# Kernel optimization log

Hardware: AMD Instinct MI355X
Metric: run time of the kernel (lower is better)

Reference implementation:

```python
import jax, jax.numpy as jnp
import numpy as np


def _min_gru_layer(h_in, Wz, bz, Wh, bh):
    # h_in: [B, T, D_in]; gates/candidate via two GEMMs
    z = jax.nn.sigmoid(jnp.einsum('btd,dh->bth', h_in, Wz) + bz)  # [B,T,H]
    h_tilde = jnp.einsum('btd,dh->bth', h_in, Wh) + bh            # [B,T,H]
    # Recurrence h_t = a_t * h_{t-1} + b_t with a_t = 1-z_t, b_t = z_t*h_tilde.
    # h_0 = 0 (frozen zeros param in the torch module), so the associative
    # scan over (a, b) directly yields h_t for t = 1..T.
    a = 1.0 - z
    b = z * h_tilde

    def combine(c1, c2):
        a1, b1 = c1
        a2, b2 = c2
        return a1 * a2, a2 * b1 + b2

    _, h = jax.lax.associative_scan(combine, (a, b), axis=1)
    return h


def setup_inputs() -> dict:
    key = jax.random.key(0)
    ks = jax.random.split(key, 8)
    B, T, Din, H, Dout = 8, 4096, 512, 1024, 512
    s_in = 1.0 / np.sqrt(Din)
    s_h = 1.0 / np.sqrt(H)
    return {
        'x':   jax.random.normal(ks[0], (B, T, Din), dtype=jnp.float32),
        'Wz0': jax.random.normal(ks[1], (Din, H), dtype=jnp.float32) * s_in,
        'bz0': jnp.zeros((H,), dtype=jnp.float32),
        'Wh0': jax.random.normal(ks[2], (Din, H), dtype=jnp.float32) * s_in,
        'bh0': jnp.zeros((H,), dtype=jnp.float32),
        'Wz1': jax.random.normal(ks[3], (H, H), dtype=jnp.float32) * s_h,
        'bz1': jnp.zeros((H,), dtype=jnp.float32),
        'Wh1': jax.random.normal(ks[4], (H, H), dtype=jnp.float32) * s_h,
        'bh1': jnp.zeros((H,), dtype=jnp.float32),
        'Wfc': jax.random.normal(ks[5], (H, Dout), dtype=jnp.float32) * s_h,
        'bfc': jnp.zeros((Dout,), dtype=jnp.float32),
    }


def reference(x, Wz0, bz0, Wh0, bh0, Wz1, bz1, Wh1, bh1, Wfc, bfc):
    h = _min_gru_layer(x, Wz0, bz0, Wh0, bh0)   # layer 0
    h = _min_gru_layer(h, Wz1, bz1, Wh1, bh1)   # layer 1
    return jnp.einsum('bth,ho->bto', h, Wfc) + bfc
```

## Files before the change

kernel.cpp:

```cpp
#include <hip/hip_runtime.h>

typedef __attribute__((ext_vector_type(4))) float fv4;
typedef __attribute__((ext_vector_type(8))) _Float16 hv8;
typedef __attribute__((ext_vector_type(4))) _Float16 hv4;
typedef __attribute__((ext_vector_type(2))) _Float16 hv2;

__device__ __forceinline__ void gload16(const void* g, void* l) {
  __builtin_amdgcn_global_load_lds(
      (const __attribute__((address_space(1))) unsigned int*)g,
      (__attribute__((address_space(3))) unsigned int*)l, 16, 0, 0);
}

struct GemmCore256 {
  const _Float16 *ap, *bp;
  size_t rstep;
  _Float16* ls;
  const _Float16 *fa, *fb;
  int wv;

  __device__ __forceinline__ void init(const _Float16* A, const _Float16* Bt,
                                       _Float16* lds, int m0, int n0, int K,
                                       int tid) {
    ls = lds;
    wv = tid >> 6;
    const int lane = tid & 63;
    const int wm = wv >> 2, wn = wv & 3;
    const int quad = lane >> 4, r = lane & 15;
    const int cg = (tid & 3) ^ ((tid >> 3) & 3);
    ap = A  + (size_t)(m0 + (tid >> 2)) * K + cg * 8;
    bp = Bt + (size_t)(n0 + (tid >> 2)) * K + cg * 8;
    rstep = (size_t)128 * K;
    const int sq = quad ^ ((r >> 1) & 3);
    fa = ls + (wm * 128 + r) * 32 + sq * 8;
    fb = ls + 8192 + (wn * 64 + r) * 32 + sq * 8;
  }

  __device__ __forceinline__ void stage4(int s) {
    _Float16* d = ls + (s & 3) * 16384 + wv * 512;
    const _Float16* a = ap + (size_t)s * 32;
    const _Float16* b = bp + (size_t)s * 32;
    gload16(a,         d);
    gload16(a + rstep, d + 4096);
    gload16(b,         d + 8192);
    gload16(b + rstep, d + 12288);
  }

  template <int VM, bool STAGE>
  __device__ __forceinline__ void body(fv4 acc[8][4], int s) {
    __builtin_amdgcn_s_barrier();
    __builtin_amdgcn_sched_barrier(0);
    if (STAGE) stage4(s + 3);
    const _Float16* fA = fa + (s & 3) * 16384;
    const _Float16* fB = fb + (s & 3) * 16384;
    hv8 a0[8], b0[4];
#pragma unroll
    for (int t = 0; t < 4; ++t) a0[t] = *(const hv8*)(fA + t * 512);
#pragma unroll
    for (int t = 0; t < 4; ++t) b0[t] = *(const hv8*)(fB + t * 512);
#pragma unroll
    for (int t = 0; t < 4; ++t) a0[t + 4] = *(const hv8*)(fA + (t + 4) * 512);
    __builtin_amdgcn_s_setprio(1);
#pragma unroll
    for (int tm = 0; tm < 4; ++tm)
#pragma unroll
      for (int tn = 0; tn < 4; ++tn)
        acc[tm][tn] = __builtin_amdgcn_mfma_f32_16x16x32_f16(a0[tm], b0[tn],
                                                             acc[tm][tn], 0, 0, 0);
#pragma unroll
    for (int tm = 0; tm < 4; ++tm)
#pragma unroll
      for (int tn = 0; tn < 4; ++tn)
        acc[tm + 4][tn] = __builtin_amdgcn_mfma_f32_16x16x32_f16(a0[tm + 4], b0[tn],
                                                                 acc[tm + 4][tn], 0, 0, 0);
    __builtin_amdgcn_s_setprio(0);
    if constexpr (VM >= 0)
      asm volatile("s_waitcnt vmcnt(%0)" :: "n"(VM) : "memory");
  }

  __device__ __forceinline__ void run(fv4 acc[8][4], int K) {
    const int ns = K >> 5;
    stage4(0); stage4(1); stage4(2);
    asm volatile("s_waitcnt vmcnt(8)" ::: "memory");
    int s = 0;
    for (; s < ns - 3; ++s) body<8, true>(acc, s);
    body<4, false>(acc, s); ++s;
    body<0, false>(acc, s); ++s;
    body<-1, false>(acc, s);
  }
};

__device__ __forceinline__ void xcd_map(int bid, int ntl2, int mt_per_x,
                                        int& m0, int& n0) {
  const int xcd = bid & 7;
  const int k2  = bid >> 3;
  m0 = (xcd * mt_per_x + (k2 >> ntl2)) * 256;
  n0 = (k2 & ((1 << ntl2) - 1)) * 256;
}

__global__ __launch_bounds__(512, 2)
void gemm_gate(const _Float16* __restrict__ A, const _Float16* __restrict__ Btf,
               _Float16* __restrict__ zh2,
               float* __restrict__ cA, float* __restrict__ cB,
               const float* __restrict__ bz, const float* __restrict__ bh,
               int K, int ntl2, int mt_per_x) {
  __shared__ _Float16 lds[4 * 16384];
  const int tid  = threadIdx.x;
  const int lane = tid & 63;
  const int wave = tid >> 6;
  const int wm = wave >> 2, wn = wave & 3;
  const int quad = lane >> 4, r = lane & 15;
  int m0, n0;
  xcd_map(blockIdx.x, ntl2, mt_per_x, m0, n0);

  GemmCore256 core;
  core.init(A, Btf, lds, m0, n0, K, tid);
  fv4 acc[8][4] = {};
  core.run(acc, K);

  const int jb   = (n0 + wn * 64) >> 1;
  const int row0 = m0 + wm * 128 + quad * 4;
  const int cb   = (m0 >> 6) + wm * 2;
#pragma unroll
  for (int tn = 0; tn < 2; ++tn) {
    const int j = jb + tn * 16 + r;
    const float bzv = bz[j];
    const float bhv = bh[j];
#pragma unroll
    for (int tg = 0; tg < 2; ++tg) {
      float qA[4], qB[4];
#pragma unroll
      for (int tq = 0; tq < 4; ++tq) {
        const int tm = tg * 4 + tq;
        float sA = 1.0f, sB = 0.0f;
#pragma unroll
        for (int r2 = 0; r2 < 4; ++r2) {
          const float zpre = acc[tm][tn][r2] + bzv;
          const float hpre = acc[tm][tn + 2][r2] + bhv;
          const float z = 1.0f / (1.0f + __expf(-zpre));
          const _Float16 a16 = (_Float16)(1.0f - z);
          const _Float16 b16 = (_Float16)(z * hpre);
          hv2 ab = {a16, b16};
          *(hv2*)(zh2 + ((size_t)(row0 + tm * 16 + r2) * 1024 + j) * 2) = ab;
          const float af = (float)a16, bf = (float)b16;
          sB = af * sB + bf;
          sA = sA * af;
        }
        qA[tq] = sA; qB[tq] = sB;
      }
#pragma unroll
      for (int tq = 0; tq < 4; ++tq) {
        float Av = qA[tq], Bv = qB[tq];
        float Ap = __shfl_up(Av, 16, 64);
        float Bp = __shfl_up(Bv, 16, 64);
        if (quad >= 1) { Bv = Av * Bp + Bv; Av = Ap * Av; }
        Ap = __shfl_up(Av, 32, 64);
        Bp = __shfl_up(Bv, 32, 64);
        if (quad >= 2) { Bv = Av * Bp + Bv; Av = Ap * Av; }
        qA[tq] = Av; qB[tq] = Bv;
      }
      if (quad == 3) {
        float CA = 1.0f, CB = 0.0f;
#pragma unroll
        for (int tq = 0; tq < 4; ++tq) { CB = qA[tq] * CB + qB[tq]; CA *= qA[tq]; }
        cA[(size_t)(cb + tg) * 1024 + j] = CA;
        cB[(size_t)(cb + tg) * 1024 + j] = CB;
      }
    }
  }
}

__global__ __launch_bounds__(512, 2)
void gemm_f16_bt(const _Float16* __restrict__ A, const _Float16* __restrict__ Bt,
                 float* __restrict__ C, const float* __restrict__ bias,
                 int N, int K, int ntl2, int mt_per_x) {
  __shared__ _Float16 lds[4 * 16384];
  const int tid  = threadIdx.x;
  const int lane = tid & 63;
  const int wave = tid >> 6;
  const int wm = wave >> 2, wn = wave & 3;
  const int quad = lane >> 4, r = lane & 15;
  int m0, n0;
  xcd_map(blockIdx.x, ntl2, mt_per_x, m0, n0);

  GemmCore256 core;
  core.init(A, Bt, lds, m0, n0, K, tid);
  fv4 acc[8][4] = {};
  core.run(acc, K);

  const int col0 = n0 + wn * 64 + r;
  const int row0 = m0 + wm * 128 + quad * 4;
#pragma unroll
  for (int tn = 0; tn < 4; ++tn) {
    const int col = col0 + tn * 16;
    const float bs = bias[col];
#pragma unroll
    for (int tm = 0; tm < 8; ++tm) {
#pragma unroll
      for (int r2 = 0; r2 < 4; ++r2) {
        C[(size_t)(row0 + tm * 16 + r2) * N + col] = acc[tm][tn][r2] + bs;
      }
    }
  }
}

__global__ void cvt_f16(const float* __restrict__ x, _Float16* __restrict__ y) {
  size_t i = ((size_t)blockIdx.x * 256 + threadIdx.x) * 4;
  fv4 v = *(const fv4*)(x + i);
  *(hv4*)(y + i) = __builtin_convertvector(v, hv4);
}

__global__ void transpose_cvt(const float* __restrict__ W, _Float16* __restrict__ Wt,
                              int K, int N, int mult, int off) {
  __shared__ float tile[32][33];
  const int tx = threadIdx.x, ty = threadIdx.y;
  const int n  = blockIdx.x * 32 + tx;
  const int kb = blockIdx.y * 32;
  for (int i = ty; i < 32; i += 8)
    tile[i][tx] = W[(size_t)(kb + i) * N + n];
  __syncthreads();
  const int k = kb + tx;
  for (int i = ty; i < 32; i += 8)
    Wt[(size_t)(blockIdx.x * mult + off + i) * K + k] = (_Float16)tile[tx][i];
}

__global__ void scan_phaseB(const float* __restrict__ cA, const float* __restrict__ cB,
                            float* __restrict__ hcy) {
  const int gtid = blockIdx.x * 256 + threadIdx.x;
  const int lane = gtid & 63;
  const int wid  = gtid >> 6;
  const int h  = (wid & 255) * 4;
  const int bb = wid >> 8;
  const size_t o = (size_t)(bb * 64 + lane) * 1024 + h;
  fv4 Aa = *(const fv4*)(cA + o);
  fv4 Bv = *(const fv4*)(cB + o);
#pragma unroll
  for (int d = 1; d < 64; d <<= 1) {
    fv4 Ap, Bp;
#pragma unroll
    for (int k = 0; k < 4; ++k) {
      Ap[k] = __shfl_up(Aa[k], d, 64);
      Bp[k] = __shfl_up(Bv[k], d, 64);
    }
    if (lane >= d) {
      Bv = Aa * Bp + Bv;
      Aa = Ap * Aa;
    }
  }
  fv4 hc;
#pragma unroll
  for (int k = 0; k < 4; ++k) hc[k] = __shfl_up(Bv[k], 1, 64);
  if (lane == 0) { hc.x = 0.f; hc.y = 0.f; hc.z = 0.f; hc.w = 0.f; }
  *(fv4*)(hcy + o) = hc;
}

__global__ void scan_phaseC(const _Float16* __restrict__ zh2,
                            const float* __restrict__ hcy,
                            _Float16* __restrict__ hout) {
  const int idx = blockIdx.x * 256 + threadIdx.x;
  const int h  = (idx & 255) * 4;
  const int c  = (idx >> 8) & 63;
  const int bb = idx >> 14;
  const size_t base = ((size_t)(bb * 4096 + c * 64) * 1024 + h) * 2;
  const size_t ob   = (size_t)(bb * 4096 + c * 64) * 1024 + h;
  const size_t o    = (size_t)(bb * 64 + c) * 1024 + h;
  fv4 hc = *(const fv4*)(hcy + o);
#pragma unroll 4
  for (int t = 0; t < 64; ++t) {
    hv8 v = *(const hv8*)(zh2 + base + (size_t)t * 2048);
    fv4 av = __builtin_convertvector(__builtin_shufflevector(v, v, 0, 2, 4, 6), fv4);
    fv4 bv = __builtin_convertvector(__builtin_shufflevector(v, v, 1, 3, 5, 7), fv4);
    hc = av * hc + bv;
    *(hv4*)(hout + ob + (size_t)t * 1024) = __builtin_convertvector(hc, hv4);
  }
}

extern "C" void kernel_launch(void* const* d_in, const int* in_sizes, int n_in,
                              void* d_out, int out_size, void* d_ws, size_t ws_size,
                              hipStream_t stream) {
  const float* x   = (const float*)d_in[0];
  const float* Wz0 = (const float*)d_in[1];
  const float* bz0 = (const float*)d_in[2];
  const float* Wh0 = (const float*)d_in[3];
  const float* bh0 = (const float*)d_in[4];
  const float* Wz1 = (const float*)d_in[5];
  const float* bz1 = (const float*)d_in[6];
  const float* Wh1 = (const float*)d_in[7];
  const float* bh1 = (const float*)d_in[8];
  const float* Wfc = (const float*)d_in[9];
  const float* bfc = (const float*)d_in[10];

  const int Mrows = 32768;
  const int H = 1024, Din = 512, Dout = 512;

  char* w = (char*)d_ws;
  _Float16* zh2   = (_Float16*)w; w += (size_t)Mrows * 2 * H * 2;
  _Float16* hx    = (_Float16*)w; w += (size_t)Mrows * H * 2;
  _Float16* Wzh0t = (_Float16*)w; w += (size_t)2 * H * Din * 2;
  _Float16* Wzh1t = (_Float16*)w; w += (size_t)2 * H * H * 2;
  _Float16* Wft   = (_Float16*)w; w += (size_t)Dout * H * 2;
  float*    cA    = (float*)w;    w += (size_t)8 * 64 * H * 4;
  float*    cB    = (float*)w;    w += (size_t)8 * 64 * H * 4;
  float*    hcy   = (float*)w;    w += (size_t)8 * 64 * H * 4;
  _Float16* Xb    = hx;

  cvt_f16<<<Mrows * Din / 1024, 256, 0, stream>>>(x, Xb);
  transpose_cvt<<<dim3(H / 32, Din / 32), dim3(32, 8), 0, stream>>>(Wz0, Wzh0t, Din, H, 64, 0);
  transpose_cvt<<<dim3(H / 32, Din / 32), dim3(32, 8), 0, stream>>>(Wh0, Wzh0t, Din, H, 64, 32);
  transpose_cvt<<<dim3(H / 32, H / 32),   dim3(32, 8), 0, stream>>>(Wz1, Wzh1t, H, H, 64, 0);
  transpose_cvt<<<dim3(H / 32, H / 32),   dim3(32, 8), 0, stream>>>(Wh1, Wzh1t, H, H, 64, 32);
  transpose_cvt<<<dim3(Dout / 32, H / 32), dim3(32, 8), 0, stream>>>(Wfc, Wft, H, Dout, 32, 0);

  gemm_gate<<<1024, 512, 0, stream>>>(Xb, Wzh0t, zh2, cA, cB, bz0, bh0, Din, 3, 16);
  scan_phaseB<<<512, 256, 0, stream>>>(cA, cB, hcy);
  scan_phaseC<<<512, 256, 0, stream>>>(zh2, hcy, hx);

  gemm_gate<<<1024, 512, 0, stream>>>(hx, Wzh1t, zh2, cA, cB, bz1, bh1, H, 3, 16);
  scan_phaseB<<<512, 256, 0, stream>>>(cA, cB, hcy);
  scan_phaseC<<<512, 256, 0, stream>>>(zh2, hcy, hx);

  gemm_f16_bt<<<256, 512, 0, stream>>>(hx, Wft, (float*)d_out, bfc, Dout, H, 1, 16);
}
```

Baseline: 503.8 us.

## Prefetch next stage A fragments from LDS and move vmcnt wait before barrier

Restructures the GEMM main loop so half of the A-operand fragments for the next K-step are read from LDS during the current step, using two ping-pong register sets. The global-to-LDS issue and vmcnt wait now come before the barrier, and the loop is unrolled by two with a dedicated last-step body. The aim is to hide LDS read latency behind MFMA work. In exchange it raises register pressure and changes barrier and wait ordering, which could cause stalls or race risk with 4-stage LDS buffering.

Measured after the change: 511.7 us. No clear change (+1.6%).

```diff
diff --git a/kernel.cpp b/kernel.cpp
--- a/kernel.cpp
+++ b/kernel.cpp
@@ -45,47 +45,87 @@
     gload16(b + rstep, d + 12288);
   }
 
+  __device__ __forceinline__ void readA03(hv8 (&a)[4], int s) {
+    const _Float16* fA = fa + (s & 3) * 16384;
+#pragma unroll
+    for (int t = 0; t < 4; ++t) a[t] = *(const hv8*)(fA + t * 512);
+  }
+
   template <int VM, bool STAGE>
-  __device__ __forceinline__ void body(fv4 acc[8][4], int s) {
+  __device__ __forceinline__ void body(fv4 acc[8][4], hv8 (&nxt)[4],
+                                       hv8 (&cur)[4], int s) {
+    if (STAGE) stage4(s + 3);
+    if constexpr (VM >= 0)
+      asm volatile("s_waitcnt vmcnt(%0)" :: "n"(VM) : "memory");
     __builtin_amdgcn_s_barrier();
-    __builtin_amdgcn_sched_barrier(0);
-    if (STAGE) stage4(s + 3);
+    asm volatile("" ::: "memory");
     const _Float16* fA = fa + (s & 3) * 16384;
     const _Float16* fB = fb + (s & 3) * 16384;
-    hv8 a0[8], b0[4];
-#pragma unroll
-    for (int t = 0; t < 4; ++t) a0[t] = *(const hv8*)(fA + t * 512);
+    hv8 b0[4], a47[4];
 #pragma unroll
     for (int t = 0; t < 4; ++t) b0[t] = *(const hv8*)(fB + t * 512);
 #pragma unroll
-    for (int t = 0; t < 4; ++t) a0[t + 4] = *(const hv8*)(fA + (t + 4) * 512);
+    for (int t = 0; t < 4; ++t) a47[t] = *(const hv8*)(fA + (t + 4) * 512);
+    readA03(nxt, s + 1);
     __builtin_amdgcn_s_setprio(1);
 #pragma unroll
     for (int tm = 0; tm < 4; ++tm)
 #pragma unroll
       for (int tn = 0; tn < 4; ++tn)
-        acc[tm][tn] = __builtin_amdgcn_mfma_f32_16x16x32_f16(a0[tm], b0[tn],
+        acc[tm][tn] = __builtin_amdgcn_mfma_f32_16x16x32_f16(cur[tm], b0[tn],
                                                              acc[tm][tn], 0, 0, 0);
 #pragma unroll
     for (int tm = 0; tm < 4; ++tm)
 #pragma unroll
       for (int tn = 0; tn < 4; ++tn)
-        acc[tm + 4][tn] = __builtin_amdgcn_mfma_f32_16x16x32_f16(a0[tm + 4], b0[tn],
+        acc[tm + 4][tn] = __builtin_amdgcn_mfma_f32_16x16x32_f16(a47[tm], b0[tn],
                                                                  acc[tm + 4][tn], 0, 0, 0);
     __builtin_amdgcn_s_setprio(0);
-    if constexpr (VM >= 0)
-      asm volatile("s_waitcnt vmcnt(%0)" :: "n"(VM) : "memory");
+  }
+
+  __device__ __forceinline__ void bodyLast(fv4 acc[8][4], hv8 (&cur)[4], int s) {
+    __builtin_amdgcn_s_barrier();
+    asm volatile("" ::: "memory");
+    const _Float16* fA = fa + (s & 3) * 16384;
+    const _Float16* fB = fb + (s & 3) * 16384;
+    hv8 b0[4], a47[4];
+#pragma unroll
+    for (int t = 0; t < 4; ++t) b0[t] = *(const hv8*)(fB + t * 512);
+#pragma unroll
+    for (int t = 0; t < 4; ++t) a47[t] = *(const hv8*)(fA + (t + 4) * 512);
+    __builtin_amdgcn_s_setprio(1);
+#pragma unroll
+    for (int tm = 0; tm < 4; ++tm)
+#pragma unroll
+      for (int tn = 0; tn < 4; ++tn)
+        acc[tm][tn] = __builtin_amdgcn_mfma_f32_16x16x32_f16(cur[tm], b0[tn],
+                                                             acc[tm][tn], 0, 0, 0);
+#pragma unroll
+    for (int tm = 0; tm < 4; ++tm)
+#pragma unroll
+      for (int tn = 0; tn < 4; ++tn)
+        acc[tm + 4][tn] = __builtin_amdgcn_mfma_f32_16x16x32_f16(a47[tm], b0[tn],
+                                                                 acc[tm + 4][tn], 0, 0, 0);
+    __builtin_amdgcn_s_setprio(0);
   }
 
   __device__ __forceinline__ void run(fv4 acc[8][4], int K) {
     const int ns = K >> 5;
     stage4(0); stage4(1); stage4(2);
     asm volatile("s_waitcnt vmcnt(8)" ::: "memory");
+    __builtin_amdgcn_s_barrier();
+    asm volatile("" ::: "memory");
+    hv8 p0[4], p1[4];
+    readA03(p0, 0);
     int s = 0;
-    for (; s < ns - 3; ++s) body<8, true>(acc, s);
-    body<4, false>(acc, s); ++s;
-    body<0, false>(acc, s); ++s;
-    body<-1, false>(acc, s);
+    for (; s < ns - 4; s += 2) {
+      body<8, true>(acc, p1, p0, s);
+      body<8, true>(acc, p0, p1, s + 1);
+    }
+    body<8, true >(acc, p1, p0, ns - 4);
+    body<4, false>(acc, p0, p1, ns - 3);
+    body<0, false>(acc, p1, p0, ns - 2);
+    bodyLast(acc, p1, ns - 1);
   }
 };
 
```

## Shrink GEMM tiles to 256x128 with 4 waves and 3-stage LDS pipeline

Applied to the files above, without the earlier changes.

Changes the GEMM blocks from 256x256 tiles with 8 waves and 4 LDS stages to 256x128 tiles with 4 waves and 3 LDS stages. The grid doubles and LDS per block falls, so more blocks can be resident per CU. The wait-for-loads is moved to the start of each step, before the barrier, and the next prefetch is issued after the fragment reads. Each block loads more bytes per flop, and the prefetch depth is one stage shallower.

Result: slower. 522.4 us (+3.7%).

```diff
diff --git a/kernel.cpp b/kernel.cpp
--- a/kernel.cpp
+++ b/kernel.cpp
@@ -11,7 +11,7 @@
       (__attribute__((address_space(3))) unsigned int*)l, 16, 0, 0);
 }
 
-struct GemmCore256 {
+struct GemmCore128 {
   const _Float16 *ap, *bp;
   size_t rstep;
   _Float16* ls;
@@ -24,34 +24,38 @@
     ls = lds;
     wv = tid >> 6;
     const int lane = tid & 63;
-    const int wm = wv >> 2, wn = wv & 3;
+    const int wm = wv >> 1, wn = wv & 1;
     const int quad = lane >> 4, r = lane & 15;
-    const int cg = (tid & 3) ^ ((tid >> 3) & 3);
-    ap = A  + (size_t)(m0 + (tid >> 2)) * K + cg * 8;
-    bp = Bt + (size_t)(n0 + (tid >> 2)) * K + cg * 8;
-    rstep = (size_t)128 * K;
+    const int cg = (lane & 3) ^ ((lane >> 3) & 3);
+    const int rb = wv * 16 + (lane >> 2);
+    ap = A  + (size_t)(m0 + rb) * K + cg * 8;
+    bp = Bt + (size_t)(n0 + rb) * K + cg * 8;
+    rstep = (size_t)64 * K;
     const int sq = quad ^ ((r >> 1) & 3);
     fa = ls + (wm * 128 + r) * 32 + sq * 8;
     fb = ls + 8192 + (wn * 64 + r) * 32 + sq * 8;
   }
 
-  __device__ __forceinline__ void stage4(int s) {
-    _Float16* d = ls + (s & 3) * 16384 + wv * 512;
+  __device__ __forceinline__ void stage(int s) {
+    _Float16* d = ls + (s % 3) * 12288 + wv * 512;
     const _Float16* a = ap + (size_t)s * 32;
     const _Float16* b = bp + (size_t)s * 32;
-    gload16(a,         d);
-    gload16(a + rstep, d + 4096);
-    gload16(b,         d + 8192);
-    gload16(b + rstep, d + 12288);
+    gload16(a,             d);
+    gload16(a + rstep,     d + 2048);
+    gload16(a + 2 * rstep, d + 4096);
+    gload16(a + 3 * rstep, d + 6144);
+    gload16(b,             d + 8192);
+    gload16(b + rstep,     d + 10240);
   }
 
   template <int VM, bool STAGE>
   __device__ __forceinline__ void body(fv4 acc[8][4], int s) {
+    asm volatile("s_waitcnt vmcnt(%0)" :: "n"(VM) : "memory");
     __builtin_amdgcn_s_barrier();
-    __builtin_amdgcn_sched_barrier(0);
-    if (STAGE) stage4(s + 3);
-    const _Float16* fA = fa + (s & 3) * 16384;
-    const _Float16* fB = fb + (s & 3) * 16384;
+    asm volatile("" ::: "memory");
+    const int sl = s % 3;
+    const _Float16* fA = fa + sl * 12288;
+    const _Float16* fB = fb + sl * 12288;
     hv8 a0[8], b0[4];
 #pragma unroll
     for (int t = 0; t < 4; ++t) a0[t] = *(const hv8*)(fA + t * 512);
@@ -59,6 +63,7 @@
     for (int t = 0; t < 4; ++t) b0[t] = *(const hv8*)(fB + t * 512);
 #pragma unroll
     for (int t = 0; t < 4; ++t) a0[t + 4] = *(const hv8*)(fA + (t + 4) * 512);
+    if (STAGE) stage(s + 2);
     __builtin_amdgcn_s_setprio(1);
 #pragma unroll
     for (int tm = 0; tm < 4; ++tm)
@@ -73,19 +78,15 @@
         acc[tm + 4][tn] = __builtin_amdgcn_mfma_f32_16x16x32_f16(a0[tm + 4], b0[tn],
                                                                  acc[tm + 4][tn], 0, 0, 0);
     __builtin_amdgcn_s_setprio(0);
-    if constexpr (VM >= 0)
-      asm volatile("s_waitcnt vmcnt(%0)" :: "n"(VM) : "memory");
   }
 
   __device__ __forceinline__ void run(fv4 acc[8][4], int K) {
     const int ns = K >> 5;
-    stage4(0); stage4(1); stage4(2);
-    asm volatile("s_waitcnt vmcnt(8)" ::: "memory");
+    stage(0); stage(1);
     int s = 0;
-    for (; s < ns - 3; ++s) body<8, true>(acc, s);
-    body<4, false>(acc, s); ++s;
-    body<0, false>(acc, s); ++s;
-    body<-1, false>(acc, s);
+    for (; s <= ns - 3; ++s) body<6, true>(acc, s);
+    body<6, false>(acc, s); ++s;
+    body<0, false>(acc, s);
   }
 };
 
@@ -94,25 +95,25 @@
   const int xcd = bid & 7;
   const int k2  = bid >> 3;
   m0 = (xcd * mt_per_x + (k2 >> ntl2)) * 256;
-  n0 = (k2 & ((1 << ntl2) - 1)) * 256;
-}
-
-__global__ __launch_bounds__(512, 2)
+  n0 = (k2 & ((1 << ntl2) - 1)) * 128;
+}
+
+__global__ __launch_bounds__(256, 2)
 void gemm_gate(const _Float16* __restrict__ A, const _Float16* __restrict__ Btf,
                _Float16* __restrict__ zh2,
                float* __restrict__ cA, float* __restrict__ cB,
                const float* __restrict__ bz, const float* __restrict__ bh,
                int K, int ntl2, int mt_per_x) {
-  __shared__ _Float16 lds[4 * 16384];
+  __shared__ _Float16 lds[3 * 12288];
   const int tid  = threadIdx.x;
   const int lane = tid & 63;
   const int wave = tid >> 6;
-  const int wm = wave >> 2, wn = wave & 3;
+  const int wm = wave >> 1, wn = wave & 1;
   const int quad = lane >> 4, r = lane & 15;
   int m0, n0;
   xcd_map(blockIdx.x, ntl2, mt_per_x, m0, n0);
 
-  GemmCore256 core;
+  GemmCore128 core;
   core.init(A, Btf, lds, m0, n0, K, tid);
   fv4 acc[8][4] = {};
   core.run(acc, K);
@@ -169,20 +170,20 @@
   }
 }
 
-__global__ __launch_bounds__(512, 2)
+__global__ __launch_bounds__(256, 2)
 void gemm_f16_bt(const _Float16* __restrict__ A, const _Float16* __restrict__ Bt,
                  float* __restrict__ C, const float* __restrict__ bias,
                  int N, int K, int ntl2, int mt_per_x) {
-  __shared__ _Float16 lds[4 * 16384];
+  __shared__ _Float16 lds[3 * 12288];
   const int tid  = threadIdx.x;
   const int lane = tid & 63;
   const int wave = tid >> 6;
-  const int wm = wave >> 2, wn = wave & 3;
+  const int wm = wave >> 1, wn = wave & 1;
   const int quad = lane >> 4, r = lane & 15;
   int m0, n0;
   xcd_map(blockIdx.x, ntl2, mt_per_x, m0, n0);
 
-  GemmCore256 core;
+  GemmCore128 core;
   core.init(A, Bt, lds, m0, n0, K, tid);
   fv4 acc[8][4] = {};
   core.run(acc, K);
@@ -310,13 +311,13 @@
   transpose_cvt<<<dim3(H / 32, H / 32),   dim3(32, 8), 0, stream>>>(Wh1, Wzh1t, H, H, 64, 32);
   transpose_cvt<<<dim3(Dout / 32, H / 32), dim3(32, 8), 0, stream>>>(Wfc, Wft, H, Dout, 32, 0);
 
-  gemm_gate<<<1024, 512, 0, stream>>>(Xb, Wzh0t, zh2, cA, cB, bz0, bh0, Din, 3, 16);
+  gemm_gate<<<2048, 256, 0, stream>>>(Xb, Wzh0t, zh2, cA, cB, bz0, bh0, Din, 4, 16);
   scan_phaseB<<<512, 256, 0, stream>>>(cA, cB, hcy);
   scan_phaseC<<<512, 256, 0, stream>>>(zh2, hcy, hx);
 
-  gemm_gate<<<1024, 512, 0, stream>>>(hx, Wzh1t, zh2, cA, cB, bz1, bh1, H, 3, 16);
+  gemm_gate<<<2048, 256, 0, stream>>>(hx, Wzh1t, zh2, cA, cB, bz1, bh1, H, 4, 16);
   scan_phaseB<<<512, 256, 0, stream>>>(cA, cB, hcy);
   scan_phaseC<<<512, 256, 0, stream>>>(zh2, hcy, hx);
 
-  gemm_f16_bt<<<256, 512, 0, stream>>>(hx, Wft, (float*)d_out, bfc, Dout, H, 1, 16);
-}
+  gemm_f16_bt<<<512, 256, 0, stream>>>(hx, Wft, (float*)d_out, bfc, Dout, H, 2, 16);
+}
```

## Use 4-wave 256x256 GEMM blocks with 128x128 per-wave tiles

Applied to the files above, without the earlier changes.

The GEMM block drops from 8 waves to 4 waves, and each wave now computes a 128x128 sub-tile (8x8 MFMA accumulators) instead of 128x64. The goal is more MFMA work per LDS fragment load and fewer waves contending for LDS bandwidth. The vmcnt wait moves before the barrier, and each thread now issues 8 global-to-LDS loads per stage. In exchange, each wave holds 256 accumulator registers, which pushes against the register limit and lowers occupancy to one block per CU. The gate epilogue indexing is reworked to fit the wider per-wave column span.

New measurement: 549.6 us. 1.09x slower.

```diff
diff --git a/kernel.cpp b/kernel.cpp
--- a/kernel.cpp
+++ b/kernel.cpp
@@ -11,7 +11,7 @@
       (__attribute__((address_space(3))) unsigned int*)l, 16, 0, 0);
 }
 
-struct GemmCore256 {
+struct GemmCoreFat {
   const _Float16 *ap, *bp;
   size_t rstep;
   _Float16* ls;
@@ -24,68 +24,60 @@
     ls = lds;
     wv = tid >> 6;
     const int lane = tid & 63;
-    const int wm = wv >> 2, wn = wv & 3;
+    const int wm = wv >> 1, wn = wv & 1;
     const int quad = lane >> 4, r = lane & 15;
     const int cg = (tid & 3) ^ ((tid >> 3) & 3);
     ap = A  + (size_t)(m0 + (tid >> 2)) * K + cg * 8;
     bp = Bt + (size_t)(n0 + (tid >> 2)) * K + cg * 8;
-    rstep = (size_t)128 * K;
+    rstep = (size_t)64 * K;
     const int sq = quad ^ ((r >> 1) & 3);
     fa = ls + (wm * 128 + r) * 32 + sq * 8;
-    fb = ls + 8192 + (wn * 64 + r) * 32 + sq * 8;
-  }
-
-  __device__ __forceinline__ void stage4(int s) {
+    fb = ls + 8192 + (wn * 128 + r) * 32 + sq * 8;
+  }
+
+  __device__ __forceinline__ void stage8(int s) {
     _Float16* d = ls + (s & 3) * 16384 + wv * 512;
     const _Float16* a = ap + (size_t)s * 32;
     const _Float16* b = bp + (size_t)s * 32;
-    gload16(a,         d);
-    gload16(a + rstep, d + 4096);
-    gload16(b,         d + 8192);
-    gload16(b + rstep, d + 12288);
+#pragma unroll
+    for (int k = 0; k < 4; ++k)
+      gload16(a + (size_t)k * rstep, d + k * 2048);
+#pragma unroll
+    for (int k = 0; k < 4; ++k)
+      gload16(b + (size_t)k * rstep, d + 8192 + k * 2048);
   }
 
   template <int VM, bool STAGE>
-  __device__ __forceinline__ void body(fv4 acc[8][4], int s) {
+  __device__ __forceinline__ void body(fv4 acc[8][8], int s) {
+    asm volatile("s_waitcnt vmcnt(%0)" :: "n"(VM) : "memory");
     __builtin_amdgcn_s_barrier();
-    __builtin_amdgcn_sched_barrier(0);
-    if (STAGE) stage4(s + 3);
+    asm volatile("" ::: "memory");
+    if (STAGE) stage8(s + 3);
     const _Float16* fA = fa + (s & 3) * 16384;
     const _Float16* fB = fb + (s & 3) * 16384;
-    hv8 a0[8], b0[4];
-#pragma unroll
-    for (int t = 0; t < 4; ++t) a0[t] = *(const hv8*)(fA + t * 512);
-#pragma unroll
-    for (int t = 0; t < 4; ++t) b0[t] = *(const hv8*)(fB + t * 512);
-#pragma unroll
-    for (int t = 0; t < 4; ++t) a0[t + 4] = *(const hv8*)(fA + (t + 4) * 512);
+    hv8 a[8], b[8];
+#pragma unroll
+    for (int t = 0; t < 8; ++t) a[t] = *(const hv8*)(fA + t * 512);
+#pragma unroll
+    for (int t = 0; t < 8; ++t) b[t] = *(const hv8*)(fB + t * 512);
     __builtin_amdgcn_s_setprio(1);
 #pragma unroll
-    for (int tm = 0; tm < 4; ++tm)
-#pragma unroll
-      for (int tn = 0; tn < 4; ++tn)
-        acc[tm][tn] = __builtin_amdgcn_mfma_f32_16x16x32_f16(a0[tm], b0[tn],
+    for (int tm = 0; tm < 8; ++tm)
+#pragma unroll
+      for (int tn = 0; tn < 8; ++tn)
+        acc[tm][tn] = __builtin_amdgcn_mfma_f32_16x16x32_f16(a[tm], b[tn],
                                                              acc[tm][tn], 0, 0, 0);
-#pragma unroll
-    for (int tm = 0; tm < 4; ++tm)
-#pragma unroll
-      for (int tn = 0; tn < 4; ++tn)
-        acc[tm + 4][tn] = __builtin_amdgcn_mfma_f32_16x16x32_f16(a0[tm + 4], b0[tn],
-                                                                 acc[tm + 4][tn], 0, 0, 0);
     __builtin_amdgcn_s_setprio(0);
-    if constexpr (VM >= 0)
-      asm volatile("s_waitcnt vmcnt(%0)" :: "n"(VM) : "memory");
-  }
-
-  __device__ __forceinline__ void run(fv4 acc[8][4], int K) {
+  }
+
+  __device__ __forceinline__ void run(fv4 acc[8][8], int K) {
     const int ns = K >> 5;
-    stage4(0); stage4(1); stage4(2);
-    asm volatile("s_waitcnt vmcnt(8)" ::: "memory");
+    stage8(0); stage8(1); stage8(2);
     int s = 0;
-    for (; s < ns - 3; ++s) body<8, true>(acc, s);
-    body<4, false>(acc, s); ++s;
-    body<0, false>(acc, s); ++s;
-    body<-1, false>(acc, s);
+    for (; s < ns - 3; ++s) body<16, true>(acc, s);
+    body<16, false>(acc, s); ++s;
+    body<8,  false>(acc, s); ++s;
+    body<0,  false>(acc, s);
   }
 };
 
@@ -97,7 +89,7 @@
   n0 = (k2 & ((1 << ntl2) - 1)) * 256;
 }
 
-__global__ __launch_bounds__(512, 2)
+__global__ __launch_bounds__(256, 1)
 void gemm_gate(const _Float16* __restrict__ A, const _Float16* __restrict__ Btf,
                _Float16* __restrict__ zh2,
                float* __restrict__ cA, float* __restrict__ cB,
@@ -107,69 +99,72 @@
   const int tid  = threadIdx.x;
   const int lane = tid & 63;
   const int wave = tid >> 6;
-  const int wm = wave >> 2, wn = wave & 3;
+  const int wm = wave >> 1, wn = wave & 1;
   const int quad = lane >> 4, r = lane & 15;
   int m0, n0;
   xcd_map(blockIdx.x, ntl2, mt_per_x, m0, n0);
 
-  GemmCore256 core;
+  GemmCoreFat core;
   core.init(A, Btf, lds, m0, n0, K, tid);
-  fv4 acc[8][4] = {};
+  fv4 acc[8][8] = {};
   core.run(acc, K);
 
-  const int jb   = (n0 + wn * 64) >> 1;
+  const int jb   = (n0 + wn * 128) >> 1;
   const int row0 = m0 + wm * 128 + quad * 4;
   const int cb   = (m0 >> 6) + wm * 2;
 #pragma unroll
-  for (int tn = 0; tn < 2; ++tn) {
-    const int j = jb + tn * 16 + r;
-    const float bzv = bz[j];
-    const float bhv = bh[j];
-#pragma unroll
-    for (int tg = 0; tg < 2; ++tg) {
-      float qA[4], qB[4];
-#pragma unroll
-      for (int tq = 0; tq < 4; ++tq) {
-        const int tm = tg * 4 + tq;
-        float sA = 1.0f, sB = 0.0f;
-#pragma unroll
-        for (int r2 = 0; r2 < 4; ++r2) {
-          const float zpre = acc[tm][tn][r2] + bzv;
-          const float hpre = acc[tm][tn + 2][r2] + bhv;
-          const float z = 1.0f / (1.0f + __expf(-zpre));
-          const _Float16 a16 = (_Float16)(1.0f - z);
-          const _Float16 b16 = (_Float16)(z * hpre);
-          hv2 ab = {a16, b16};
-          *(hv2*)(zh2 + ((size_t)(row0 + tm * 16 + r2) * 1024 + j) * 2) = ab;
-          const float af = (float)a16, bf = (float)b16;
-          sB = af * sB + bf;
-          sA = sA * af;
+  for (int g = 0; g < 2; ++g) {
+#pragma unroll
+    for (int u = 0; u < 2; ++u) {
+      const int j = jb + g * 32 + u * 16 + r;
+      const float bzv = bz[j];
+      const float bhv = bh[j];
+#pragma unroll
+      for (int tg = 0; tg < 2; ++tg) {
+        float qA[4], qB[4];
+#pragma unroll
+        for (int tq = 0; tq < 4; ++tq) {
+          const int tm = tg * 4 + tq;
+          float sA = 1.0f, sB = 0.0f;
+#pragma unroll
+          for (int r2 = 0; r2 < 4; ++r2) {
+            const float zpre = acc[tm][g * 4 + u][r2] + bzv;
+            const float hpre = acc[tm][g * 4 + u + 2][r2] + bhv;
+            const float z = 1.0f / (1.0f + __expf(-zpre));
+            const _Float16 a16 = (_Float16)(1.0f - z);
+            const _Float16 b16 = (_Float16)(z * hpre);
+            hv2 ab = {a16, b16};
+            *(hv2*)(zh2 + ((size_t)(row0 + tm * 16 + r2) * 1024 + j) * 2) = ab;
+            const float af = (float)a16, bf = (float)b16;
+            sB = af * sB + bf;
+            sA = sA * af;
+          }
+          qA[tq] = sA; qB[tq] = sB;
         }
-        qA[tq] = sA; qB[tq] = sB;
-      }
-#pragma unroll
-      for (int tq = 0; tq < 4; ++tq) {
-        float Av = qA[tq], Bv = qB[tq];
-        float Ap = __shfl_up(Av, 16, 64);
-        float Bp = __shfl_up(Bv, 16, 64);
-        if (quad >= 1) { Bv = Av * Bp + Bv; Av = Ap * Av; }
-        Ap = __shfl_up(Av, 32, 64);
-        Bp = __shfl_up(Bv, 32, 64);
-        if (quad >= 2) { Bv = Av * Bp + Bv; Av = Ap * Av; }
-        qA[tq] = Av; qB[tq] = Bv;
-      }
-      if (quad == 3) {
-        float CA = 1.0f, CB = 0.0f;
-#pragma unroll
-        for (int tq = 0; tq < 4; ++tq) { CB = qA[tq] * CB + qB[tq]; CA *= qA[tq]; }
-        cA[(size_t)(cb + tg) * 1024 + j] = CA;
-        cB[(size_t)(cb + tg) * 1024 + j] = CB;
+#pragma unroll
+        for (int tq = 0; tq < 4; ++tq) {
+          float Av = qA[tq], Bv = qB[tq];
+          float Ap = __shfl_up(Av, 16, 64);
+          float Bp = __shfl_up(Bv, 16, 64);
+          if (quad >= 1) { Bv = Av * Bp + Bv; Av = Ap * Av; }
+          Ap = __shfl_up(Av, 32, 64);
+          Bp = __shfl_up(Bv, 32, 64);
+          if (quad >= 2) { Bv = Av * Bp + Bv; Av = Ap * Av; }
+          qA[tq] = Av; qB[tq] = Bv;
+        }
+        if (quad == 3) {
+          float CA = 1.0f, CB = 0.0f;
+#pragma unroll
+          for (int tq = 0; tq < 4; ++tq) { CB = qA[tq] * CB + qB[tq]; CA *= qA[tq]; }
+          cA[(size_t)(cb + tg) * 1024 + j] = CA;
+          cB[(size_t)(cb + tg) * 1024 + j] = CB;
+        }
       }
     }
   }
 }
 
-__global__ __launch_bounds__(512, 2)
+__global__ __launch_bounds__(256, 1)
 void gemm_f16_bt(const _Float16* __restrict__ A, const _Float16* __restrict__ Bt,
                  float* __restrict__ C, const float* __restrict__ bias,
                  int N, int K, int ntl2, int mt_per_x) {
@@ -177,20 +172,20 @@
   const int tid  = threadIdx.x;
   const int lane = tid & 63;
   const int wave = tid >> 6;
-  const int wm = wave >> 2, wn = wave & 3;
+  const int wm = wave >> 1, wn = wave & 1;
   const int quad = lane >> 4, r = lane & 15;
   int m0, n0;
   xcd_map(blockIdx.x, ntl2, mt_per_x, m0, n0);
 
-  GemmCore256 core;
+  GemmCoreFat core;
   core.init(A, Bt, lds, m0, n0, K, tid);
-  fv4 acc[8][4] = {};
+  fv4 acc[8][8] = {};
   core.run(acc, K);
 
-  const int col0 = n0 + wn * 64 + r;
+  const int col0 = n0 + wn * 128 + r;
   const int row0 = m0 + wm * 128 + quad * 4;
 #pragma unroll
-  for (int tn = 0; tn < 4; ++tn) {
+  for (int tn = 0; tn < 8; ++tn) {
     const int col = col0 + tn * 16;
     const float bs = bias[col];
 #pragma unroll
@@ -310,13 +305,13 @@
   transpose_cvt<<<dim3(H / 32, H / 32),   dim3(32, 8), 0, stream>>>(Wh1, Wzh1t, H, H, 64, 32);
   transpose_cvt<<<dim3(Dout / 32, H / 32), dim3(32, 8), 0, stream>>>(Wfc, Wft, H, Dout, 32, 0);
 
-  gemm_gate<<<1024, 512, 0, stream>>>(Xb, Wzh0t, zh2, cA, cB, bz0, bh0, Din, 3, 16);
+  gemm_gate<<<1024, 256, 0, stream>>>(Xb, Wzh0t, zh2, cA, cB, bz0, bh0, Din, 3, 16);
   scan_phaseB<<<512, 256, 0, stream>>>(cA, cB, hcy);
   scan_phaseC<<<512, 256, 0, stream>>>(zh2, hcy, hx);
 
-  gemm_gate<<<1024, 512, 0, stream>>>(hx, Wzh1t, zh2, cA, cB, bz1, bh1, H, 3, 16);
+  gemm_gate<<<1024, 256, 0, stream>>>(hx, Wzh1t, zh2, cA, cB, bz1, bh1, H, 3, 16);
   scan_phaseB<<<512, 256, 0, stream>>>(cA, cB, hcy);
   scan_phaseC<<<512, 256, 0, stream>>>(zh2, hcy, hx);
 
-  gemm_f16_bt<<<256, 512, 0, stream>>>(hx, Wft, (float*)d_out, bfc, Dout, H, 1, 16);
-}
+  gemm_f16_bt<<<256, 256, 0, stream>>>(hx, Wft, (float*)d_out, bfc, Dout, H, 1, 16);
+}
```
